# Optimization experiments

Measured on AMD Instinct MI355X. Metric: run time of the kernel, lower is better.

## Reference

```python
import jax, jax.numpy as jnp
import numpy as np

B, S, D, H, K = 1, 4096, 1024, 16, 64


def setup_inputs() -> dict:
    key = jax.random.key(0)
    ks = jax.random.split(key, 5)
    x = jax.random.normal(ks[0], (B, S, D), dtype=jnp.float32)
    wq = jax.random.normal(ks[1], (D, H, K), dtype=jnp.float32) / np.sqrt(D)
    wk = jax.random.normal(ks[2], (D, H, K), dtype=jnp.float32) / np.sqrt(D)
    wv = jax.random.normal(ks[3], (D, H, K), dtype=jnp.float32) / np.sqrt(D)
    wo = jax.random.normal(ks[4], (H, K, D), dtype=jnp.float32) / np.sqrt(H * K)
    bq = jnp.zeros((H, K), dtype=jnp.float32)
    bk = jnp.zeros((H, K), dtype=jnp.float32)
    bv = jnp.zeros((H, K), dtype=jnp.float32)
    bo = jnp.zeros((D,), dtype=jnp.float32)
    return {"x": x, "wq": wq, "bq": bq, "wk": wk, "bk": bk,
            "wv": wv, "bv": bv, "wo": wo, "bo": bo, "is_causal": 1}


def reference(x, wq, bq, wk, bk, wv, bv, wo, bo, is_causal):
    # QKV projections: [B,S,D] x [D,H,K] -> [B,S,H,K]
    q = jnp.einsum("bsd,dhk->bshk", x, wq) + bq
    k = jnp.einsum("bsd,dhk->bshk", x, wk) + bk
    v = jnp.einsum("bsd,dhk->bshk", x, wv) + bv
    # scores: [B,H,Q,KV], scaled by 1/sqrt(head_dim)
    scores = jnp.einsum("bqhk,bvhk->bhqv", q, k) / jnp.sqrt(jnp.float32(K))
    if is_causal:
        qpos = jnp.arange(S)[:, None]  # query position
        kpos = jnp.arange(S)[None, :]  # key position
        mask = (qpos >= kpos).astype(scores.dtype)  # [Q,KV]
        scores = scores - 1e9 * (1.0 - mask)
    probs = jax.nn.softmax(scores, axis=-1)
    # weighted values: [B,S,H,K]
    vals = jnp.einsum("bhqv,bvhk->bqhk", probs, v)
    # output projection: [B,S,H,K] x [H,K,D] -> [B,S,D]
    out = jnp.einsum("bqhk,hkd->bqd", vals, wo) + bo
    return out
```

## Files before the change

### kernel.cpp

```cpp
#include <hip/hip_runtime.h>

typedef _Float16 f16;
typedef f16 f16x8 __attribute__((ext_vector_type(8)));
typedef f16 f16x4 __attribute__((ext_vector_type(4)));
typedef float f32x2 __attribute__((ext_vector_type(2)));
typedef float f32x4 __attribute__((ext_vector_type(4)));
typedef float f32x16 __attribute__((ext_vector_type(16)));
typedef unsigned u32;

#define MFMA16(a, b, c) __builtin_amdgcn_mfma_f32_16x16x32_f16((a), (b), (c), 0, 0, 0)
#define MFMA32(a, b, c) __builtin_amdgcn_mfma_f32_32x32x16_f16((a), (b), (c), 0, 0, 0)

#define QSCL 0.18033688011f

#define WAITV(N) asm volatile("s_waitcnt vmcnt(" #N ")" ::: "memory")
#define BAR()                          \
  {                                    \
    __builtin_amdgcn_s_barrier();      \
    __builtin_amdgcn_sched_barrier(0); \
  }

__device__ __forceinline__ void gll16(const void* g, void* l) {
  __builtin_amdgcn_global_load_lds(
      (__attribute__((address_space(1))) unsigned int*)(void*)(g),
      (__attribute__((address_space(3))) unsigned int*)(l), 16, 0, 0);
}

__device__ __forceinline__ float ex2(float x) {
  float r;
  asm("v_exp_f32 %0, %1" : "=v"(r) : "v"(x));
  return r;
}

__device__ __forceinline__ void plswap(u32& a, u32& b) {
  asm("s_nop 1\n\tv_permlane32_swap_b32 %0, %1\n\ts_nop 1" : "+v"(a), "+v"(b));
}

__device__ __forceinline__ void plswap2(u32& a, u32& b, u32& c, u32& d) {
  asm("s_nop 1\n\tv_permlane32_swap_b32 %0, %1\n\tv_permlane32_swap_b32 %2, %3\n\ts_nop 1"
      : "+v"(a), "+v"(b), "+v"(c), "+v"(d));
}

__device__ __forceinline__ u32 pk16(float lo, float hi) {
  __fp16 h2[2];
  *(decltype(__builtin_amdgcn_cvt_pkrtz(0.f, 0.f))*)h2 =
      __builtin_amdgcn_cvt_pkrtz(lo, hi);
  return *(u32*)h2;
}

__global__ void k_prep(const float* __restrict__ x, f16* __restrict__ xb,
                       const float* __restrict__ wq, const float* __restrict__ wk,
                       const float* __restrict__ wv, const float* __restrict__ wo,
                       f16* __restrict__ wqkvT, f16* __restrict__ woT) {
  __shared__ float tile[64][65];
  const int bid = blockIdx.x;
  if (bid < 4096) {
    const int i = bid * 256 + threadIdx.x;
    float4 v = reinterpret_cast<const float4*>(x)[i];
    f16x4 o = {(f16)v.x, (f16)v.y, (f16)v.z, (f16)v.w};
    reinterpret_cast<f16x4*>(xb)[i] = o;
    return;
  }
  const int tb = bid - 4096;
  const int which = tb >> 8;
  const int bidx = tb & 255;
  const float* src = which == 0 ? wq : which == 1 ? wk : which == 2 ? wv : wo;
  f16* dst = which == 0 ? wqkvT
             : which == 1 ? wqkvT + (size_t)1024 * 1024
             : which == 2 ? wqkvT + (size_t)2048 * 1024
                          : woT;
  const int bc = bidx & 15, br = bidx >> 4;
  const int r0 = br << 6, c0 = bc << 6;
  const int tr = threadIdx.x >> 6, tc = threadIdx.x & 63;
#pragma unroll
  for (int p = 0; p < 16; ++p)
    tile[p * 4 + tr][tc] = src[(size_t)(r0 + p * 4 + tr) * 1024 + c0 + tc];
  __syncthreads();
#pragma unroll
  for (int p = 0; p < 16; ++p)
    dst[(size_t)(c0 + p * 4 + tr) * 1024 + r0 + tc] = (f16)tile[tc][p * 4 + tr];
}

template <int MODE, int NFR, int PAIR>
__global__ __launch_bounds__(256, 3) void k_gemm(
    const f16* __restrict__ A, const f16* __restrict__ Bt, int nbm, int Kd,
    const float* __restrict__ bias0, const float* __restrict__ bias1,
    const float* __restrict__ bias2,
    f16* __restrict__ Qo, f16* __restrict__ Ko, f16* __restrict__ Vo,
    float* __restrict__ Fo) {
  constexpr int TSZ = 8192 + NFR * 2048;
  constexpr int NBUF = PAIR ? 4 : 3;
  __shared__ __align__(16) char smem[NBUF * TSZ];
  const int tid = threadIdx.x;
  const int wid = tid >> 6, lane = tid & 63;
  const int r = lane & 15, t = lane >> 4;
  const int bm = blockIdx.x % nbm, bn = blockIdx.x / nbm;
  const int m0 = bm << 7, n0 = bn * (NFR * 32);
  const int wr = wid >> 1, wc = wid & 1;

  const f32x4 vz = {0.f, 0.f, 0.f, 0.f};
  f32x4 acc[4][NFR];
#pragma unroll
  for (int m = 0; m < 4; ++m)
#pragma unroll
    for (int n = 0; n < NFR; ++n) acc[m][n] = vz;

  const int srow = tid >> 2;
  const int scb = (((tid & 3) ^ ((tid >> 3) & 3)) << 4);
  const size_t ldb = (size_t)Kd * 2;
  const char* Ab = (const char*)A + (size_t)m0 * ldb + scb;
  const char* Bb = (const char*)Bt + (size_t)n0 * ldb + scb;

  auto issue = [&](int kt, int buf) {
    const size_t kb = (size_t)kt << 6;
    char* base = smem + buf * TSZ;
    gll16(Ab + (size_t)srow * ldb + kb, base + wid * 1024);
    gll16(Ab + (size_t)(srow + 64) * ldb + kb, base + 4096 + wid * 1024);
    gll16(Bb + (size_t)srow * ldb + kb, base + 8192 + wid * 1024);
    if (NFR == 4)
      gll16(Bb + (size_t)(srow + 64) * ldb + kb, base + 8192 + 4096 + wid * 1024);
  };

  const int swz = ((r >> 1) & 3) << 4;

  auto comp = [&](int buf) {
    const char* base = smem + buf * TSZ;
    f16x8 af[4], bg[NFR];
#pragma unroll
    for (int m = 0; m < 4; ++m)
      af[m] = *(const f16x8*)(base + ((wr * 64 + m * 16 + r) * 64 +
                                      ((t * 16) ^ swz)));
#pragma unroll
    for (int n = 0; n < NFR; ++n)
      bg[n] = *(const f16x8*)(base + 8192 +
                              ((wc * (NFR * 16) + n * 16 + r) * 64 +
                               ((t * 16) ^ swz)));
    __builtin_amdgcn_s_setprio(1);
#pragma unroll
    for (int m = 0; m < 4; ++m)
#pragma unroll
      for (int n = 0; n < NFR; ++n) acc[m][n] = MFMA16(af[m], bg[n], acc[m][n]);
    __builtin_amdgcn_s_setprio(0);
  };

  const int nk = Kd >> 5;
  if (PAIR) {
    issue(0, 0);
    issue(1, 1);
    const int nsup = nk >> 1;
    for (int T = 0; T < nsup; ++T) {
      WAITV(0);
      BAR();
      if (T + 1 < nsup) {
        issue(2 * T + 2, (2 * T + 2) & 3);
        issue(2 * T + 3, (2 * T + 3) & 3);
      }
      comp((2 * T) & 3);
      comp((2 * T + 1) & 3);
    }
  } else {
    issue(0, 0);
    issue(1, 1);
    int b = 0, bi = 2;
    for (int kt = 0; kt < nk; ++kt) {
      if (kt + 1 < nk) {
        if (NFR == 4) {
          WAITV(4);
        } else {
          WAITV(3);
        }
      } else {
        WAITV(0);
      }
      BAR();
      if (kt + 2 < nk) issue(kt + 2, bi);
      comp(b);
      b = (b == 2) ? 0 : b + 1;
      bi = (bi == 2) ? 0 : bi + 1;
    }
  }

#pragma unroll
  for (int m = 0; m < 4; ++m) {
    const int row0 = m0 + wr * 64 + m * 16 + t * 4;
#pragma unroll
    for (int n = 0; n < NFR; ++n) {
      const int gc = n0 + wc * (NFR * 16) + n * 16 + r;
      if (MODE == 0) {
        const float b2 = gc < 1024 ? bias0[gc]
                                   : (gc < 2048 ? bias1[gc - 1024] : bias2[gc - 2048]);
        float v[4];
#pragma unroll
        for (int i = 0; i < 4; ++i) v[i] = acc[m][n][i] + b2;
        if (gc < 1024) {
#pragma unroll
          for (int i = 0; i < 4; ++i)
            Qo[(size_t)(row0 + i) * 1024 + gc] = (f16)(v[i] * QSCL);
        } else if (gc < 2048) {
#pragma unroll
          for (int i = 0; i < 4; ++i)
            Ko[(size_t)(row0 + i) * 1024 + (gc - 1024)] = (f16)v[i];
        } else {
          f16x4 pk = {(f16)v[0], (f16)v[1], (f16)v[2], (f16)v[3]};
          *(f16x4*)(Vo + (size_t)(gc - 2048) * 4096 + row0) = pk;
        }
      } else {
        const float b2 = bias0[gc];
#pragma unroll
        for (int i = 0; i < 4; ++i)
          Fo[(size_t)(row0 + i) * 1024 + gc] = acc[m][n][i] + b2;
      }
    }
  }
}

__global__ __launch_bounds__(512, 4) void k_fattn(
    const f16* __restrict__ Q, const f16* __restrict__ Kb,
    const f16* __restrict__ Vt, f16* __restrict__ vals,
    const int* __restrict__ causp) {
  __shared__ uint4 ldsv[4128];
  char* lds = (char*)ldsv;
  const int tid = threadIdx.x;
  const int W = tid >> 6, lane = tid & 63;
  const int l31 = lane & 31, hi = lane >> 5;
  const int wq = W >> 1, wkv = W & 1;
  const int h = blockIdx.x & 15;
  const int idx = blockIdx.x >> 4;
  const int qt = idx < 16 ? 31 - idx : idx - 16;
  const int cz = *causp;
  const int Tmax = cz ? qt : 31;
  const int dw = wq - wkv;
  const int jmax_w = cz ? (2 * qt + (dw >= 2 ? 1 : 0) - (dw < 0 ? 1 : 0)) : 63;
  const bool maskd = cz && ((dw & 1) == 0);

  const size_t qrow = (size_t)((qt << 7) + (wq << 5) + l31) * 1024 + h * 64;
  f16x8 qf[4];
#pragma unroll
  for (int s = 0; s < 4; ++s) qf[s] = *(const f16x8*)(Q + qrow + 16 * s + 8 * hi);

  f32x16 o0, o1, zv;
#pragma unroll
  for (int e = 0; e < 16; ++e) { o0[e] = 0.f; o1[e] = 0.f; zv[e] = 0.f; }
  float Ls = 0.f;

  const int srw = lane >> 3, sch = lane & 7;
  const int ssw = (sch ^ srw) << 3;
  const char* kcur =
      (const char*)(Kb + (size_t)(8 * W + srw) * 1024 + h * 64 + ssw);
  const char* vcur =
      (const char*)(Vt + (size_t)(h * 64 + 8 * W + srw) * 4096 + ssw);

  auto issue = [&](int buf) {
    char* base = lds + buf * 16384 + W * 1024;
    gll16(kcur, base);
    gll16(vcur, base + 8192);
    kcur += (size_t)64 * 2048;
    vcur += 128;
  };

  const int krow = (wkv << 5) + l31, ksw = krow & 7;
  const int vsw = l31 & 7;
  int koff[4];
#pragma unroll
  for (int s = 0; s < 4; ++s)
    koff[s] = krow * 128 + (((2 * s + hi) ^ ksw) << 4);
  int voffA[2], voffB[2];
#pragma unroll
  for (int ks = 0; ks < 2; ++ks) {
    const int cl = 4 * wkv + 2 * ks + hi;
    voffA[ks] = l31 * 128 + ((cl ^ vsw) << 4);
    voffB[ks] = (32 + l31) * 128 + ((cl ^ vsw) << 4);
  }

  auto qk = [&](const char* Kbase) -> f32x16 {
    f16x8 af[4];
#pragma unroll
    for (int s = 0; s < 4; ++s)
      af[s] = *(const f16x8*)(Kbase + koff[s]);
    __builtin_amdgcn_s_setprio(1);
    f32x16 sc = MFMA32(af[0], qf[0], zv);
#pragma unroll
    for (int s = 1; s < 4; ++s) sc = MFMA32(af[s], qf[s], sc);
    __builtin_amdgcn_s_setprio(0);
    return sc;
  };

  auto fin = [&](int j, const char* Kbase, f32x16& sc) {
    const char* Vbase = Kbase + 8192;
    if (maskd && j == jmax_w) {
#pragma unroll
      for (int e = 0; e < 16; ++e) {
        const int kvr = (e & 3) + 8 * (e >> 2) + 4 * hi;
        if (kvr > l31) sc[e] = -1e9f;
      }
    }
    f32x2 p2[8];
#pragma unroll
    for (int e = 0; e < 8; ++e) {
      f32x2 t;
      t[0] = ex2(sc[2 * e]);
      t[1] = ex2(sc[2 * e + 1]);
      p2[e] = t;
    }
    {
      f32x2 a0 = p2[0] + p2[1];
      f32x2 a1 = p2[2] + p2[3];
      f32x2 a2 = p2[4] + p2[5];
      f32x2 a3 = p2[6] + p2[7];
      f32x2 b0 = a0 + a1;
      f32x2 b1 = a2 + a3;
      f32x2 c = b0 + b1;
      float s = c[0] + c[1];
      union { float f; u32 u; } ua, ub;
      ua.f = s; ub.f = s;
      plswap(ua.u, ub.u);
      Ls += ua.f + ub.f;
    }
#pragma unroll
    for (int ks = 0; ks < 2; ++ks) {
      u32 c0 = pk16(p2[4 * ks + 0][0], p2[4 * ks + 0][1]);
      u32 c1 = pk16(p2[4 * ks + 1][0], p2[4 * ks + 1][1]);
      u32 c2 = pk16(p2[4 * ks + 2][0], p2[4 * ks + 2][1]);
      u32 c3 = pk16(p2[4 * ks + 3][0], p2[4 * ks + 3][1]);
      plswap2(c0, c2, c1, c3);
      union { u32 w[4]; f16x8 v; } pa;
      pa.w[0] = c0; pa.w[1] = c1; pa.w[2] = c2; pa.w[3] = c3;
      const f16x8 vf0 = *(const f16x8*)(Vbase + voffA[ks]);
      const f16x8 vf1 = *(const f16x8*)(Vbase + voffB[ks]);
      __builtin_amdgcn_s_setprio(1);
      o0 = MFMA32(pa.v, vf0, o0);
      o1 = MFMA32(pa.v, vf1, o1);
      __builtin_amdgcn_s_setprio(0);
    }
  };

  issue(0);
  issue(1);

  for (int T = 0; T <= Tmax; ++T) {
    BAR();
    if (T < Tmax) {
      const int nb = 2 * ((T + 1) & 1);
      issue(nb);
      issue(nb + 1);
      WAITV(4);
    } else {
      WAITV(0);
    }
    const int cb = 2 * (T & 1);
    const char* bA = lds + cb * 16384;
    const char* bB = lds + (cb + 1) * 16384;
    const int jA = 2 * T, jB = 2 * T + 1;
    if (jB <= jmax_w) {
      f32x16 scA = qk(bA);
      f32x16 scB = qk(bB);
      fin(jA, bA, scA);
      fin(jB, bB, scB);
    } else if (jA <= jmax_w) {
      f32x16 scA = qk(bA);
      fin(jA, bA, scA);
    }
  }
  __syncthreads();

  float* obuf = (float*)lds;
  float* lsbuf = (float*)(lds + 32768);
  if (hi == 0) lsbuf[wq * 64 + wkv * 32 + l31] = Ls;
  if (wkv == 1) {
    float* base = obuf + wq * 2048;
#pragma unroll
    for (int dblk = 0; dblk < 2; ++dblk)
#pragma unroll
      for (int rg = 0; rg < 4; ++rg) {
        const f32x16& o = dblk ? o1 : o0;
        f32x4 t = {o[rg * 4 + 0], o[rg * 4 + 1], o[rg * 4 + 2], o[rg * 4 + 3]};
        *(f32x4*)(base + ((dblk * 4 + rg) * 64 + lane) * 4) = t;
      }
  }
  __syncthreads();
  if (wkv == 0) {
    float* base = obuf + wq * 2048;
#pragma unroll
    for (int dblk = 0; dblk < 2; ++dblk)
#pragma unroll
      for (int rg = 0; rg < 4; ++rg) {
        f32x4 t = *(f32x4*)(base + ((dblk * 4 + rg) * 64 + lane) * 4);
        f32x16& o = dblk ? o1 : o0;
#pragma unroll
        for (int i = 0; i < 4; ++i) o[rg * 4 + i] += t[i];
      }
    float inv[16];
#pragma unroll
    for (int e = 0; e < 16; ++e) {
      const int q = (e & 3) + 8 * (e >> 2) + 4 * hi;
      inv[e] = 1.0f / (lsbuf[wq * 64 + q] + lsbuf[wq * 64 + 32 + q]);
    }
    const int row0 = (qt << 7) + (wq << 5);
#pragma unroll
    for (int dblk = 0; dblk < 2; ++dblk) {
      const f32x16& o = dblk ? o1 : o0;
      const int col = h * 64 + 32 * dblk + l31;
#pragma unroll
      for (int e = 0; e < 16; ++e) {
        const int rr = row0 + (e & 3) + 8 * (e >> 2) + 4 * hi;
        vals[(size_t)rr * 1024 + col] = (f16)(o[e] * inv[e]);
      }
    }
  }
}

extern "C" void kernel_launch(void* const* d_in, const int* in_sizes, int n_in,
                              void* d_out, int out_size, void* d_ws, size_t ws_size,
                              hipStream_t stream) {
  const float* x = (const float*)d_in[0];
  const float* wq = (const float*)d_in[1];
  const float* bq = (const float*)d_in[2];
  const float* wk = (const float*)d_in[3];
  const float* bk = (const float*)d_in[4];
  const float* wv = (const float*)d_in[5];
  const float* bv = (const float*)d_in[6];
  const float* wo = (const float*)d_in[7];
  const float* bo = (const float*)d_in[8];
  const int* caus = (const int*)d_in[9];
  float* out = (float*)d_out;

  f16* xb = (f16*)d_ws;
  f16* wqkvT = xb + (size_t)4096 * 1024;
  f16* woT = wqkvT + (size_t)3072 * 1024;
  f16* Qb = woT + (size_t)1024 * 1024;
  f16* Kbuf = Qb + (size_t)4096 * 1024;
  f16* Vt = Kbuf + (size_t)4096 * 1024;
  f16* vals = Vt + (size_t)4096 * 1024;

  k_prep<<<5120, 256, 0, stream>>>(x, xb, wq, wk, wv, wo, wqkvT, woT);
  k_gemm<0, 4, 0><<<32 * 24, 256, 0, stream>>>(xb, wqkvT, 32, 1024, bq, bk, bv,
                                               Qb, Kbuf, Vt, nullptr);
  k_fattn<<<512, 512, 0, stream>>>(Qb, Kbuf, Vt, vals, caus);
  k_gemm<1, 2, 1><<<32 * 16, 256, 0, stream>>>(vals, woT, 32, 1024, bo, nullptr,
                                               nullptr, nullptr, nullptr,
                                               nullptr, out);
}
```

Measured before the change: 117.6 us.

## Pair complementary causal query tiles in one 1024-thread attention block sharing K/V loads

The flash attention kernel now launches 256 blocks of 1024 threads. Each block handles two query tiles of the same head, a long one (31-pi) and a short one (pi), and the two halves share the K/V tiles staged in LDS. K loads are issued by the first 8 waves and V loads by the last 8, so each wave issues half as many global-to-LDS copies. The change is meant to balance causal work per block and cut redundant K/V traffic, at the cost of more LDS per block, fewer resident blocks per CU, and the short tile's waves idling through the long tile's iterations.

After: 117.1 us. No clear change (-0.4%).

```diff
diff --git a/kernel.cpp b/kernel.cpp
--- a/kernel.cpp
+++ b/kernel.cpp
@@ -214,21 +214,23 @@
   }
 }
 
-__global__ __launch_bounds__(512, 4) void k_fattn(
+__global__ __launch_bounds__(1024, 4) void k_fattn(
     const f16* __restrict__ Q, const f16* __restrict__ Kb,
     const f16* __restrict__ Vt, f16* __restrict__ vals,
     const int* __restrict__ causp) {
-  __shared__ uint4 ldsv[4128];
+  __shared__ uint4 ldsv[4224];
   char* lds = (char*)ldsv;
   const int tid = threadIdx.x;
   const int W = tid >> 6, lane = tid & 63;
   const int l31 = lane & 31, hi = lane >> 5;
-  const int wq = W >> 1, wkv = W & 1;
+  const int h2 = W >> 3;
+  const int Wl = W & 7;
+  const int wq = Wl >> 1, wkv = Wl & 1;
   const int h = blockIdx.x & 15;
-  const int idx = blockIdx.x >> 4;
-  const int qt = idx < 16 ? 31 - idx : idx - 16;
+  const int pi = blockIdx.x >> 4;
+  const int qt = h2 == 0 ? 31 - pi : pi;
   const int cz = *causp;
-  const int Tmax = cz ? qt : 31;
+  const int Tmax = cz ? (31 - pi) : 31;
   const int dw = wq - wkv;
   const int jmax_w = cz ? (2 * qt + (dw >= 2 ? 1 : 0) - (dw < 0 ? 1 : 0)) : 63;
   const bool maskd = cz && ((dw & 1) == 0);
@@ -245,17 +247,22 @@
 
   const int srw = lane >> 3, sch = lane & 7;
   const int ssw = (sch ^ srw) << 3;
-  const char* kcur =
-      (const char*)(Kb + (size_t)(8 * W + srw) * 1024 + h * 64 + ssw);
-  const char* vcur =
-      (const char*)(Vt + (size_t)(h * 64 + 8 * W + srw) * 4096 + ssw);
+  const char* gcur;
+  size_t gstep;
+  int sdst;
+  if (W < 8) {
+    gcur = (const char*)(Kb + (size_t)(8 * W + srw) * 1024 + h * 64 + ssw);
+    gstep = (size_t)64 * 2048;
+    sdst = W * 1024;
+  } else {
+    gcur = (const char*)(Vt + (size_t)(h * 64 + 8 * (W - 8) + srw) * 4096 + ssw);
+    gstep = 128;
+    sdst = 8192 + (W - 8) * 1024;
+  }
 
   auto issue = [&](int buf) {
-    char* base = lds + buf * 16384 + W * 1024;
-    gll16(kcur, base);
-    gll16(vcur, base + 8192);
-    kcur += (size_t)64 * 2048;
-    vcur += 128;
+    gll16(gcur, lds + buf * 16384 + sdst);
+    gcur += gstep;
   };
 
   const int krow = (wkv << 5) + l31, ksw = krow & 7;
@@ -343,7 +350,7 @@
       const int nb = 2 * ((T + 1) & 1);
       issue(nb);
       issue(nb + 1);
-      WAITV(4);
+      WAITV(2);
     } else {
       WAITV(0);
     }
@@ -363,8 +370,8 @@
   }
   __syncthreads();
 
-  float* obuf = (float*)lds;
-  float* lsbuf = (float*)(lds + 32768);
+  float* obuf = (float*)(lds + h2 * 32768);
+  float* lsbuf = (float*)(lds + 65536 + h2 * 1024);
   if (hi == 0) lsbuf[wq * 64 + wkv * 32 + l31] = Ls;
   if (wkv == 1) {
     float* base = obuf + wq * 2048;
@@ -435,7 +442,7 @@
   k_prep<<<5120, 256, 0, stream>>>(x, xb, wq, wk, wv, wo, wqkvT, woT);
   k_gemm<0, 4, 0><<<32 * 24, 256, 0, stream>>>(xb, wqkvT, 32, 1024, bq, bk, bv,
                                                Qb, Kbuf, Vt, nullptr);
-  k_fattn<<<512, 512, 0, stream>>>(Qb, Kbuf, Vt, vals, caus);
+  k_fattn<<<256, 1024, 0, stream>>>(Qb, Kbuf, Vt, vals, caus);
   k_gemm<1, 2, 1><<<32 * 16, 256, 0, stream>>>(vals, woT, 32, 1024, bo, nullptr,
                                                nullptr, nullptr, nullptr,
                                                nullptr, out);
```

## Pair complementary causal query tiles per block, each wave computing 64 query rows

Applied to the files above, without the earlier changes.

Each attention workgroup now handles two 128-row query tiles, a late one (31-b) and an early one (b), in separate wave pairs that share the same K/V LDS stream. Each wave holds 64 query rows (two 32-row MFMA groups), so every K/V fragment read from LDS is reused twice. The grid halves to 256 blocks and the occupancy hint drops from 4 to 2 to make room for the larger register footprint. The intent is to balance causal work inside a block and cut LDS traffic per FLOP. The cost is fewer blocks to spread across the GPU and lower occupancy. Waves on the short tile also sit idle while their partners finish the long one.

After: 120.2 us. +2.2%, slower.

```diff
diff --git a/kernel.cpp b/kernel.cpp
--- a/kernel.cpp
+++ b/kernel.cpp
@@ -214,34 +214,39 @@
   }
 }
 
-__global__ __launch_bounds__(512, 4) void k_fattn(
+__global__ __launch_bounds__(512, 2) void k_fattn(
     const f16* __restrict__ Q, const f16* __restrict__ Kb,
     const f16* __restrict__ Vt, f16* __restrict__ vals,
     const int* __restrict__ causp) {
-  __shared__ uint4 ldsv[4128];
+  __shared__ uint4 ldsv[4224];
   char* lds = (char*)ldsv;
   const int tid = threadIdx.x;
   const int W = tid >> 6, lane = tid & 63;
   const int l31 = lane & 31, hi = lane >> 5;
-  const int wq = W >> 1, wkv = W & 1;
+  const int wkv = W & 1, wQ = W >> 1;
+  const int qh = wQ & 1;
   const int h = blockIdx.x & 15;
-  const int idx = blockIdx.x >> 4;
-  const int qt = idx < 16 ? 31 - idx : idx - 16;
+  const int b = blockIdx.x >> 4;
+  const int qt = (wQ < 2) ? (31 - b) : b;
   const int cz = *causp;
-  const int Tmax = cz ? qt : 31;
-  const int dw = wq - wkv;
-  const int jmax_w = cz ? (2 * qt + (dw >= 2 ? 1 : 0) - (dw < 0 ? 1 : 0)) : 63;
-  const bool maskd = cz && ((dw & 1) == 0);
-
-  const size_t qrow = (size_t)((qt << 7) + (wq << 5) + l31) * 1024 + h * 64;
-  f16x8 qf[4];
-#pragma unroll
-  for (int s = 0; s < 4; ++s) qf[s] = *(const f16x8*)(Q + qrow + 16 * s + 8 * hi);
-
-  f32x16 o0, o1, zv;
-#pragma unroll
-  for (int e = 0; e < 16; ++e) { o0[e] = 0.f; o1[e] = 0.f; zv[e] = 0.f; }
-  float Ls = 0.f;
+  const int Tmax = cz ? (31 - b) : 31;
+  const int jmax_w = cz ? (2 * qt + qh) : 63;
+
+  const size_t qr0 = (size_t)((qt << 7) + (qh << 6) + l31) * 1024 + h * 64;
+  const size_t qr1 = qr0 + (size_t)32 * 1024;
+  f16x8 qf0[4], qf1[4];
+#pragma unroll
+  for (int s = 0; s < 4; ++s) {
+    qf0[s] = *(const f16x8*)(Q + qr0 + 16 * s + 8 * hi);
+    qf1[s] = *(const f16x8*)(Q + qr1 + 16 * s + 8 * hi);
+  }
+
+  f32x16 o00, o01, o10, o11, zv;
+#pragma unroll
+  for (int e = 0; e < 16; ++e) {
+    o00[e] = 0.f; o01[e] = 0.f; o10[e] = 0.f; o11[e] = 0.f; zv[e] = 0.f;
+  }
+  float Ls0 = 0.f, Ls1 = 0.f;
 
   const int srw = lane >> 3, sch = lane & 7;
   const int ssw = (sch ^ srw) << 3;
@@ -272,64 +277,81 @@
     voffB[ks] = (32 + l31) * 128 + ((cl ^ vsw) << 4);
   }
 
-  auto qk = [&](const char* Kbase) -> f32x16 {
+  auto tilec = [&](int j, const char* Kbase) {
+    if (j > jmax_w) return;
+    const char* Vbase = Kbase + 8192;
     f16x8 af[4];
 #pragma unroll
-    for (int s = 0; s < 4; ++s)
-      af[s] = *(const f16x8*)(Kbase + koff[s]);
+    for (int s = 0; s < 4; ++s) af[s] = *(const f16x8*)(Kbase + koff[s]);
     __builtin_amdgcn_s_setprio(1);
-    f32x16 sc = MFMA32(af[0], qf[0], zv);
-#pragma unroll
-    for (int s = 1; s < 4; ++s) sc = MFMA32(af[s], qf[s], sc);
+    f32x16 sc0 = MFMA32(af[0], qf0[0], zv);
+    f32x16 sc1 = MFMA32(af[0], qf1[0], zv);
+#pragma unroll
+    for (int s = 1; s < 4; ++s) {
+      sc0 = MFMA32(af[s], qf0[s], sc0);
+      sc1 = MFMA32(af[s], qf1[s], sc1);
+    }
     __builtin_amdgcn_s_setprio(0);
-    return sc;
-  };
-
-  auto fin = [&](int j, const char* Kbase, f32x16& sc) {
-    const char* Vbase = Kbase + 8192;
-    if (maskd && j == jmax_w) {
-#pragma unroll
-      for (int e = 0; e < 16; ++e) {
-        const int kvr = (e & 3) + 8 * (e >> 2) + 4 * hi;
-        if (kvr > l31) sc[e] = -1e9f;
-      }
-    }
-    f32x2 p2[8];
+    if (cz && j == jmax_w) {
+      if (wkv == 0) {
+#pragma unroll
+        for (int e = 0; e < 16; ++e) {
+          const int kvr = (e & 3) + 8 * (e >> 2) + 4 * hi;
+          if (kvr > l31) sc0[e] = -1e9f;
+        }
+      } else {
+#pragma unroll
+        for (int e = 0; e < 16; ++e) sc0[e] = -1e9f;
+#pragma unroll
+        for (int e = 0; e < 16; ++e) {
+          const int kvr = (e & 3) + 8 * (e >> 2) + 4 * hi;
+          if (kvr > l31) sc1[e] = -1e9f;
+        }
+      }
+    }
+    f32x2 p0[8], p1[8];
 #pragma unroll
     for (int e = 0; e < 8; ++e) {
-      f32x2 t;
-      t[0] = ex2(sc[2 * e]);
-      t[1] = ex2(sc[2 * e + 1]);
-      p2[e] = t;
+      f32x2 t0, t1;
+      t0[0] = ex2(sc0[2 * e]); t0[1] = ex2(sc0[2 * e + 1]);
+      t1[0] = ex2(sc1[2 * e]); t1[1] = ex2(sc1[2 * e + 1]);
+      p0[e] = t0; p1[e] = t1;
     }
     {
-      f32x2 a0 = p2[0] + p2[1];
-      f32x2 a1 = p2[2] + p2[3];
-      f32x2 a2 = p2[4] + p2[5];
-      f32x2 a3 = p2[6] + p2[7];
-      f32x2 b0 = a0 + a1;
-      f32x2 b1 = a2 + a3;
-      f32x2 c = b0 + b1;
-      float s = c[0] + c[1];
-      union { float f; u32 u; } ua, ub;
-      ua.f = s; ub.f = s;
-      plswap(ua.u, ub.u);
-      Ls += ua.f + ub.f;
+      f32x2 a0 = (p0[0] + p0[1]) + (p0[2] + p0[3]);
+      f32x2 a1 = (p0[4] + p0[5]) + (p0[6] + p0[7]);
+      f32x2 b0 = (p1[0] + p1[1]) + (p1[2] + p1[3]);
+      f32x2 b1 = (p1[4] + p1[5]) + (p1[6] + p1[7]);
+      f32x2 ca = a0 + a1, cb = b0 + b1;
+      union { float f; u32 u; } u0a, u0b, u1a, u1b;
+      u0a.f = ca[0] + ca[1]; u0b.f = u0a.f;
+      u1a.f = cb[0] + cb[1]; u1b.f = u1a.f;
+      plswap2(u0a.u, u0b.u, u1a.u, u1b.u);
+      Ls0 += u0a.f + u0b.f;
+      Ls1 += u1a.f + u1b.f;
     }
 #pragma unroll
     for (int ks = 0; ks < 2; ++ks) {
-      u32 c0 = pk16(p2[4 * ks + 0][0], p2[4 * ks + 0][1]);
-      u32 c1 = pk16(p2[4 * ks + 1][0], p2[4 * ks + 1][1]);
-      u32 c2 = pk16(p2[4 * ks + 2][0], p2[4 * ks + 2][1]);
-      u32 c3 = pk16(p2[4 * ks + 3][0], p2[4 * ks + 3][1]);
+      u32 c0 = pk16(p0[4 * ks + 0][0], p0[4 * ks + 0][1]);
+      u32 c1 = pk16(p0[4 * ks + 1][0], p0[4 * ks + 1][1]);
+      u32 c2 = pk16(p0[4 * ks + 2][0], p0[4 * ks + 2][1]);
+      u32 c3 = pk16(p0[4 * ks + 3][0], p0[4 * ks + 3][1]);
+      u32 d0 = pk16(p1[4 * ks + 0][0], p1[4 * ks + 0][1]);
+      u32 d1 = pk16(p1[4 * ks + 1][0], p1[4 * ks + 1][1]);
+      u32 d2 = pk16(p1[4 * ks + 2][0], p1[4 * ks + 2][1]);
+      u32 d3 = pk16(p1[4 * ks + 3][0], p1[4 * ks + 3][1]);
       plswap2(c0, c2, c1, c3);
-      union { u32 w[4]; f16x8 v; } pa;
-      pa.w[0] = c0; pa.w[1] = c1; pa.w[2] = c2; pa.w[3] = c3;
+      plswap2(d0, d2, d1, d3);
+      union { u32 w[4]; f16x8 v; } pa0, pa1;
+      pa0.w[0] = c0; pa0.w[1] = c1; pa0.w[2] = c2; pa0.w[3] = c3;
+      pa1.w[0] = d0; pa1.w[1] = d1; pa1.w[2] = d2; pa1.w[3] = d3;
       const f16x8 vf0 = *(const f16x8*)(Vbase + voffA[ks]);
       const f16x8 vf1 = *(const f16x8*)(Vbase + voffB[ks]);
       __builtin_amdgcn_s_setprio(1);
-      o0 = MFMA32(pa.v, vf0, o0);
-      o1 = MFMA32(pa.v, vf1, o1);
+      o00 = MFMA32(pa0.v, vf0, o00);
+      o01 = MFMA32(pa0.v, vf1, o01);
+      o10 = MFMA32(pa1.v, vf0, o10);
+      o11 = MFMA32(pa1.v, vf1, o11);
       __builtin_amdgcn_s_setprio(0);
     }
   };
@@ -348,64 +370,70 @@
       WAITV(0);
     }
     const int cb = 2 * (T & 1);
-    const char* bA = lds + cb * 16384;
-    const char* bB = lds + (cb + 1) * 16384;
-    const int jA = 2 * T, jB = 2 * T + 1;
-    if (jB <= jmax_w) {
-      f32x16 scA = qk(bA);
-      f32x16 scB = qk(bB);
-      fin(jA, bA, scA);
-      fin(jB, bB, scB);
-    } else if (jA <= jmax_w) {
-      f32x16 scA = qk(bA);
-      fin(jA, bA, scA);
-    }
+    tilec(2 * T, lds + cb * 16384);
+    tilec(2 * T + 1, lds + (cb + 1) * 16384);
   }
   __syncthreads();
 
-  float* obuf = (float*)lds;
-  float* lsbuf = (float*)(lds + 32768);
-  if (hi == 0) lsbuf[wq * 64 + wkv * 32 + l31] = Ls;
+  float* obuf = (float*)(lds + wQ * 16384);
+  float* lsbuf = (float*)(lds + 65536);
+  if (hi == 0) {
+    lsbuf[(wQ * 2 + wkv) * 64 + l31] = Ls0;
+    lsbuf[(wQ * 2 + wkv) * 64 + 32 + l31] = Ls1;
+  }
   if (wkv == 1) {
-    float* base = obuf + wq * 2048;
-#pragma unroll
-    for (int dblk = 0; dblk < 2; ++dblk)
-#pragma unroll
-      for (int rg = 0; rg < 4; ++rg) {
-        const f32x16& o = dblk ? o1 : o0;
-        f32x4 t = {o[rg * 4 + 0], o[rg * 4 + 1], o[rg * 4 + 2], o[rg * 4 + 3]};
-        *(f32x4*)(base + ((dblk * 4 + rg) * 64 + lane) * 4) = t;
+#pragma unroll
+    for (int g = 0; g < 2; ++g)
+#pragma unroll
+      for (int dblk = 0; dblk < 2; ++dblk) {
+        const f32x16& o = g == 0 ? (dblk == 0 ? o00 : o01)
+                                 : (dblk == 0 ? o10 : o11);
+#pragma unroll
+        for (int rg = 0; rg < 4; ++rg) {
+          f32x4 t = {o[rg * 4 + 0], o[rg * 4 + 1], o[rg * 4 + 2], o[rg * 4 + 3]};
+          *(f32x4*)(obuf + (((g * 2 + dblk) * 4 + rg) * 64 + lane) * 4) = t;
+        }
       }
   }
   __syncthreads();
   if (wkv == 0) {
-    float* base = obuf + wq * 2048;
-#pragma unroll
-    for (int dblk = 0; dblk < 2; ++dblk)
-#pragma unroll
-      for (int rg = 0; rg < 4; ++rg) {
-        f32x4 t = *(f32x4*)(base + ((dblk * 4 + rg) * 64 + lane) * 4);
-        f32x16& o = dblk ? o1 : o0;
-#pragma unroll
-        for (int i = 0; i < 4; ++i) o[rg * 4 + i] += t[i];
-      }
-    float inv[16];
+#pragma unroll
+    for (int g = 0; g < 2; ++g)
+#pragma unroll
+      for (int dblk = 0; dblk < 2; ++dblk) {
+        f32x16& o = g == 0 ? (dblk == 0 ? o00 : o01)
+                           : (dblk == 0 ? o10 : o11);
+#pragma unroll
+        for (int rg = 0; rg < 4; ++rg) {
+          f32x4 t =
+              *(f32x4*)(obuf + (((g * 2 + dblk) * 4 + rg) * 64 + lane) * 4);
+#pragma unroll
+          for (int i = 0; i < 4; ++i) o[rg * 4 + i] += t[i];
+        }
+      }
+    float inv0[16], inv1[16];
 #pragma unroll
     for (int e = 0; e < 16; ++e) {
       const int q = (e & 3) + 8 * (e >> 2) + 4 * hi;
-      inv[e] = 1.0f / (lsbuf[wq * 64 + q] + lsbuf[wq * 64 + 32 + q]);
-    }
-    const int row0 = (qt << 7) + (wq << 5);
-#pragma unroll
-    for (int dblk = 0; dblk < 2; ++dblk) {
-      const f32x16& o = dblk ? o1 : o0;
-      const int col = h * 64 + 32 * dblk + l31;
-#pragma unroll
-      for (int e = 0; e < 16; ++e) {
-        const int rr = row0 + (e & 3) + 8 * (e >> 2) + 4 * hi;
-        vals[(size_t)rr * 1024 + col] = (f16)(o[e] * inv[e]);
-      }
-    }
+      inv0[e] = 1.0f / (lsbuf[(wQ * 2) * 64 + q] + lsbuf[(wQ * 2 + 1) * 64 + q]);
+      inv1[e] = 1.0f /
+                (lsbuf[(wQ * 2) * 64 + 32 + q] + lsbuf[(wQ * 2 + 1) * 64 + 32 + q]);
+    }
+    const int row0 = (qt << 7) + (qh << 6);
+#pragma unroll
+    for (int g = 0; g < 2; ++g)
+#pragma unroll
+      for (int dblk = 0; dblk < 2; ++dblk) {
+        const f32x16& o = g == 0 ? (dblk == 0 ? o00 : o01)
+                                 : (dblk == 0 ? o10 : o11);
+        const int col = h * 64 + 32 * dblk + l31;
+#pragma unroll
+        for (int e = 0; e < 16; ++e) {
+          const int rr = row0 + g * 32 + (e & 3) + 8 * (e >> 2) + 4 * hi;
+          const float iv = g == 0 ? inv0[e] : inv1[e];
+          vals[(size_t)rr * 1024 + col] = (f16)(o[e] * iv);
+        }
+      }
   }
 }
 
@@ -435,7 +463,7 @@
   k_prep<<<5120, 256, 0, stream>>>(x, xb, wq, wk, wv, wo, wqkvT, woT);
   k_gemm<0, 4, 0><<<32 * 24, 256, 0, stream>>>(xb, wqkvT, 32, 1024, bq, bk, bv,
                                                Qb, Kbuf, Vt, nullptr);
-  k_fattn<<<512, 512, 0, stream>>>(Qb, Kbuf, Vt, vals, caus);
+  k_fattn<<<256, 512, 0, stream>>>(Qb, Kbuf, Vt, vals, caus);
   k_gemm<1, 2, 1><<<32 * 16, 256, 0, stream>>>(vals, woT, 32, 1024, bo, nullptr,
                                                nullptr, nullptr, nullptr,
                                                nullptr, out);
```
